# Performance work log

Measured on AMD Instinct MI355X. Metric: run time of the kernel, lower is better.

Reference implementation:

```python
import jax, jax.numpy as jnp
import numpy as np

N = 50000      # nodes
E = 800000     # edges (avg degree 16)
F_IN = 256
F_OUT = 256


def setup_inputs() -> dict:
    key = jax.random.key(0)
    ks = jax.random.split(key, 8)
    feature = jax.random.normal(ks[0], (N, F_IN), dtype=jnp.float32)
    e_w = jax.random.uniform(ks[1], (E, 1), dtype=jnp.float32)
    snorm_n = jnp.ones((N, 1), dtype=jnp.float32)
    snorm_e = jnp.ones((E, 1), dtype=jnp.float32)
    src = jax.random.randint(ks[2], (E,), 0, N, dtype=jnp.int32)
    dst = jax.random.randint(ks[3], (E,), 0, N, dtype=jnp.int32)
    scale = 1.0 / np.sqrt(F_IN)
    W_self = jax.random.normal(ks[4], (F_IN, F_OUT), dtype=jnp.float32) * scale
    W = jax.random.normal(ks[5], (F_IN, F_OUT), dtype=jnp.float32) * scale
    b = jax.random.normal(ks[6], (F_OUT,), dtype=jnp.float32) * scale
    return {"feature": feature, "e_w": e_w, "snorm_n": snorm_n,
            "snorm_e": snorm_e, "W_self": W_self, "W": W, "b": b,
            "src": src, "dst": dst}


def reference(feature, e_w, snorm_n, snorm_e, W_self, W, b, src, dst):
    n = feature.shape[0]
    ones_e = jnp.ones_like(src, dtype=feature.dtype)
    # self transform
    h_s = feature @ W_self                                   # [N, F_OUT]
    # source-side degree normalization: deg_out^{-1/2}
    out_deg = jnp.maximum(jax.ops.segment_sum(ones_e, src, num_segments=n), 1.0)
    feat = feature * (out_deg ** -0.5)[:, None]              # [N, F_IN]
    # message = h[src] * e_w, aggregated by sum into dst (u_mul_e + sum reduce)
    msgs = feat[src] * e_w                                   # [E, F_IN]
    agg = jax.ops.segment_sum(msgs, dst, num_segments=n)     # [N, F_IN]
    # neighbor transform + destination-side degree normalization
    h = agg @ W + b                                          # [N, F_OUT]
    in_deg = jnp.maximum(jax.ops.segment_sum(ones_e, dst, num_segments=n), 1.0)
    h = h * (in_deg ** -0.5)[:, None]
    return h_s + h, e_w
```

## Files before the change

kernel.cpp:

```cpp
#include <hip/hip_runtime.h>
#include <hip/hip_bf16.h>

#define N_NODES 50000
#define N_EDGES 800000
#define MP      50048
#define MAXDEG  64

#define PREP_A_BLOCKS 12512
#define EDGE_BLOCKS   3125
#define PREPW_BLOCKS  512

typedef __bf16 bf16x8_t __attribute__((ext_vector_type(8)));
typedef float  f32x4_t  __attribute__((ext_vector_type(4)));

__device__ __forceinline__ unsigned short f2bf(float x) {
  __hip_bfloat16 h = __float2bfloat16(x);
  return __builtin_bit_cast(unsigned short, h);
}
__device__ __forceinline__ float bf2f(unsigned short u) {
  unsigned int v = ((unsigned int)u) << 16;
  return __builtin_bit_cast(float, v);
}

__global__ __launch_bounds__(256) void prep_fused(
    const float* __restrict__ feature, const float* __restrict__ Wself,
    const float* __restrict__ W, const float* __restrict__ e_w,
    const int* __restrict__ src, const int* __restrict__ dst,
    unsigned short* __restrict__ Abf, unsigned short* __restrict__ Bt,
    int* __restrict__ cnt_in, int* __restrict__ cnt_out,
    unsigned int* __restrict__ bucket, float* __restrict__ out1)
{
  const int b = blockIdx.x, tid = threadIdx.x;
  if (b < PREP_A_BLOCKS) {
    int idx4 = b * 256 + tid;
    size_t base = (size_t)idx4 * 4;
    int row = (int)(base >> 8);
    ushort4 o;
    if (row < N_NODES) {
      const float4 v = *(const float4*)(feature + base);
      o.x = f2bf(v.x); o.y = f2bf(v.y); o.z = f2bf(v.z); o.w = f2bf(v.w);
    } else {
      o.x = o.y = o.z = o.w = 0;
    }
    *(ushort4*)(Abf + base) = o;
  } else if (b < PREP_A_BLOCKS + EDGE_BLOCKS) {
    int e = (b - PREP_A_BLOCKS) * 256 + tid;
    if (e < N_EDGES) {
      int s = src[e];
      int d = dst[e];
      float w = e_w[e];
      out1[e] = w;
      atomicAdd(&cnt_out[s], 1);
      int p = atomicAdd(&cnt_in[d], 1);
      if (p < MAXDEG) {
        unsigned int ent = ((unsigned int)f2bf(w) << 16) | (unsigned int)s;
        bucket[(size_t)d * MAXDEG + p] = ent;
      }
    }
  } else {
    int idx = (b - (PREP_A_BLOCKS + EDGE_BLOCKS)) * 256 + tid;
    int n = idx >> 8, k = idx & 255;
    float v = (n < 256) ? Wself[k * 256 + n] : W[k * 256 + (n - 256)];
    Bt[idx] = f2bf(v);
  }
}

__global__ __launch_bounds__(256, 2) void gemm_kernel(
    const unsigned short* __restrict__ A,
    const unsigned short* __restrict__ Bt,
    const float* __restrict__ bias,
    const int* __restrict__ cnt_in,
    const int* __restrict__ cnt_out,
    float* __restrict__ out0,
    unsigned char* __restrict__ y8)
{
  __shared__ unsigned short As[2][128 * 32];
  __shared__ unsigned short Bs[2][256 * 32];
  const int tid  = threadIdx.x;
  const int lane = tid & 63;
  const int wave = tid >> 6;
  const int m0 = blockIdx.x * 128;
  const int n0 = blockIdx.y * 256;
  const int wm = (wave & 1) * 64;
  const int wn = (wave >> 1) * 128;
  const int fr = lane & 15;
  const int fk = (lane >> 4) * 8;
  const int srow  = lane >> 2;
  const int scolb = (lane & 3) * 8;

  f32x4_t acc[4][8] = {};

  for (int k0 = 0; k0 < 256; k0 += 64) {
#pragma unroll
    for (int p = 0; p < 2; ++p) {
      int kk = k0 + p * 32;
#pragma unroll
      for (int j = 0; j < 2; ++j) {
        int rr = wave * 32 + j * 16;
        const unsigned short* ga = A + (size_t)(m0 + rr + srow) * 256 + (kk + scolb);
        __builtin_amdgcn_global_load_lds((const __attribute__((address_space(1))) void*)ga,
                                         (__attribute__((address_space(3))) void*)&As[p][rr * 32],
                                         16, 0, 0);
      }
#pragma unroll
      for (int j = 0; j < 4; ++j) {
        int rr = wave * 64 + j * 16;
        const unsigned short* gb = Bt + (size_t)(n0 + rr + srow) * 256 + (kk + scolb);
        __builtin_amdgcn_global_load_lds((const __attribute__((address_space(1))) void*)gb,
                                         (__attribute__((address_space(3))) void*)&Bs[p][rr * 32],
                                         16, 0, 0);
      }
    }
    __syncthreads();

#pragma unroll
    for (int p = 0; p < 2; ++p) {
      bf16x8_t af[4], bfr[8];
#pragma unroll
      for (int i = 0; i < 4; ++i)
        af[i]  = *(const bf16x8_t*)&As[p][(wm + i * 16 + fr) * 32 + fk];
#pragma unroll
      for (int j = 0; j < 8; ++j)
        bfr[j] = *(const bf16x8_t*)&Bs[p][(wn + j * 16 + fr) * 32 + fk];
#pragma unroll
      for (int i = 0; i < 4; ++i)
#pragma unroll
        for (int j = 0; j < 8; ++j)
          acc[i][j] = __builtin_amdgcn_mfma_f32_16x16x32_bf16(af[i], bfr[j], acc[i][j], 0, 0, 0);
    }
    __syncthreads();
  }

  if (blockIdx.y == 0) {
#pragma unroll
    for (int i = 0; i < 4; ++i) {
      int rowb = m0 + wm + i * 16 + (lane >> 4) * 4;
      float indv[4];
#pragma unroll
      for (int r = 0; r < 4; ++r) {
        int row = rowb + r;
        if (row < N_NODES) {
          int ci = cnt_in[row]; if (ci < 1) ci = 1;
          indv[r] = rsqrtf((float)ci);
        } else indv[r] = 0.f;
      }
#pragma unroll
      for (int j = 0; j < 8; ++j) {
        int col = wn + j * 16 + (lane & 15);
        float bc = bias[col];
#pragma unroll
        for (int r = 0; r < 4; ++r) {
          int row = rowb + r;
          if (row < N_NODES)
            out0[(size_t)row * 256 + col] = acc[i][j][r] + bc * indv[r];
        }
      }
    }
  } else {
#pragma unroll
    for (int i = 0; i < 4; ++i) {
      int rowb = m0 + wm + i * 16 + (lane >> 4) * 4;
      float odv[4];
#pragma unroll
      for (int r = 0; r < 4; ++r) {
        int row = rowb + r;
        if (row < N_NODES) {
          int co = cnt_out[row]; if (co < 1) co = 1;
          odv[r] = rsqrtf((float)co);
        } else odv[r] = 0.f;
      }
#pragma unroll
      for (int j = 0; j < 8; ++j) {
        int col = wn + j * 16 + (lane & 15);
#pragma unroll
        for (int r = 0; r < 4; ++r) {
          int row = rowb + r;
          if (row < N_NODES) {
            float ys = acc[i][j][r] * odv[r];
            unsigned int pk = (unsigned int)__builtin_amdgcn_cvt_pk_fp8_f32(ys, ys, 0, false);
            y8[(size_t)row * 256 + col] = (unsigned char)(pk & 0xffu);
          }
        }
      }
    }
  }
}

__global__ __launch_bounds__(256) void agg_kernel(
    const unsigned char* __restrict__ y8, const unsigned int* __restrict__ bucket,
    const int* __restrict__ cnt_in, float* __restrict__ out0)
{
  const int wave = threadIdx.x >> 6, lane = threadIdx.x & 63;
  const int node = blockIdx.x * 4 + wave;
  if (node >= N_NODES) return;
  int deg_raw = cnt_in[node];
  int deg = deg_raw > MAXDEG ? MAXDEG : deg_raw;

  unsigned int ent = 0u;
  if (lane < deg) ent = bucket[(size_t)node * MAXDEG + lane];
  float wl = bf2f((unsigned short)(ent >> 16));
  int   sl = (int)(ent & 0xffffu);

  float a0 = 0.f, a1 = 0.f, a2 = 0.f, a3 = 0.f;
  for (int b = 0; b < MAXDEG; b += 16) {
    if (b >= deg) break;
#pragma unroll
    for (int t = 0; t < 16; ++t) {
      int eb = b + t;
      int   s = __shfl(sl, eb);
      float w = __shfl(wl, eb);
      bool ok = eb < deg;
      s = ok ? s : 0;
      w = ok ? w : 0.0f;
      unsigned int u = *(const unsigned int*)(y8 + (size_t)s * 256 + lane * 4);
      a0 += w * __builtin_amdgcn_cvt_f32_fp8(u, 0);
      a1 += w * __builtin_amdgcn_cvt_f32_fp8(u, 1);
      a2 += w * __builtin_amdgcn_cvt_f32_fp8(u, 2);
      a3 += w * __builtin_amdgcn_cvt_f32_fp8(u, 3);
    }
  }

  int dn = deg_raw < 1 ? 1 : deg_raw;
  float inv = rsqrtf((float)dn);
  float4 o = *(float4*)(out0 + (size_t)node * 256 + lane * 4);
  o.x += a0 * inv; o.y += a1 * inv; o.z += a2 * inv; o.w += a3 * inv;
  *(float4*)(out0 + (size_t)node * 256 + lane * 4) = o;
}

extern "C" void kernel_launch(void* const* d_in, const int* in_sizes, int n_in,
                              void* d_out, int out_size, void* d_ws, size_t ws_size,
                              hipStream_t stream) {
  const float* feature = (const float*)d_in[0];
  const float* e_w     = (const float*)d_in[1];
  const float* W_self  = (const float*)d_in[4];
  const float* W       = (const float*)d_in[5];
  const float* bias    = (const float*)d_in[6];
  const int*   src     = (const int*)d_in[7];
  const int*   dst     = (const int*)d_in[8];

  float* out0 = (float*)d_out;
  float* out1 = out0 + (size_t)N_NODES * 256;

  char* ws = (char*)d_ws;
  int*            cnt_in  = (int*)(ws + 0);
  int*            cnt_out = (int*)(ws + 204800);
  unsigned int*   bucket  = (unsigned int*)(ws + 409600);
  unsigned short* Bt      = (unsigned short*)(ws + 13209600);
  unsigned short* Abf     = (unsigned short*)(ws + 13471744);
  unsigned char*  y8      = (unsigned char*)(ws + 39096320);

  hipMemsetAsync(ws, 0, 409600, stream);

  prep_fused<<<PREP_A_BLOCKS + EDGE_BLOCKS + PREPW_BLOCKS, 256, 0, stream>>>(
      feature, W_self, W, e_w, src, dst, Abf, Bt, cnt_in, cnt_out, bucket, out1);
  gemm_kernel<<<dim3(MP / 128, 2), 256, 0, stream>>>(Abf, Bt, bias, cnt_in, cnt_out, out0, y8);
  agg_kernel<<<(N_NODES + 3) / 4, 256, 0, stream>>>(y8, bucket, cnt_in, out0);
}
```

Baseline: 265.3 us.

## Fuse bf16 feature conversion into GEMM and co-schedule edge bucketing blocks

```diff
diff --git a/kernel.cpp b/kernel.cpp
--- a/kernel.cpp
+++ b/kernel.cpp
@@ -6,9 +6,9 @@
 #define MP      50048
 #define MAXDEG  64
 
-#define PREP_A_BLOCKS 12512
-#define EDGE_BLOCKS   3125
-#define PREPW_BLOCKS  512
+#define GEMM_BLOCKS  782
+#define EDGE_BLOCKS  782
+#define WCONV_BLOCKS 512
 
 typedef __bf16 bf16x8_t __attribute__((ext_vector_type(8)));
 typedef float  f32x4_t  __attribute__((ext_vector_type(4)));
@@ -22,86 +22,71 @@
   return __builtin_bit_cast(float, v);
 }
 
-__global__ __launch_bounds__(256) void prep_fused(
-    const float* __restrict__ feature, const float* __restrict__ Wself,
-    const float* __restrict__ W, const float* __restrict__ e_w,
-    const int* __restrict__ src, const int* __restrict__ dst,
-    unsigned short* __restrict__ Abf, unsigned short* __restrict__ Bt,
+__global__ __launch_bounds__(256) void wconv_kernel(
+    const float* __restrict__ Wself, const float* __restrict__ W,
+    unsigned short* __restrict__ Bt)
+{
+  int idx = blockIdx.x * 256 + threadIdx.x;
+  int n = idx >> 8, k = idx & 255;
+  float v = (n < 256) ? Wself[k * 256 + n] : W[k * 256 + (n - 256)];
+  Bt[idx] = f2bf(v);
+}
+
+__global__ __launch_bounds__(256, 2) void gemm_edge_kernel(
+    const float* __restrict__ feature,
+    const unsigned short* __restrict__ Bt,
+    const float* __restrict__ e_w, const int* __restrict__ src, const int* __restrict__ dst,
     int* __restrict__ cnt_in, int* __restrict__ cnt_out,
-    unsigned int* __restrict__ bucket, float* __restrict__ out1)
-{
-  const int b = blockIdx.x, tid = threadIdx.x;
-  if (b < PREP_A_BLOCKS) {
-    int idx4 = b * 256 + tid;
-    size_t base = (size_t)idx4 * 4;
-    int row = (int)(base >> 8);
-    ushort4 o;
-    if (row < N_NODES) {
-      const float4 v = *(const float4*)(feature + base);
-      o.x = f2bf(v.x); o.y = f2bf(v.y); o.z = f2bf(v.z); o.w = f2bf(v.w);
-    } else {
-      o.x = o.y = o.z = o.w = 0;
-    }
-    *(ushort4*)(Abf + base) = o;
-  } else if (b < PREP_A_BLOCKS + EDGE_BLOCKS) {
-    int e = (b - PREP_A_BLOCKS) * 256 + tid;
-    if (e < N_EDGES) {
-      int s = src[e];
-      int d = dst[e];
-      float w = e_w[e];
-      out1[e] = w;
-      atomicAdd(&cnt_out[s], 1);
-      int p = atomicAdd(&cnt_in[d], 1);
-      if (p < MAXDEG) {
-        unsigned int ent = ((unsigned int)f2bf(w) << 16) | (unsigned int)s;
-        bucket[(size_t)d * MAXDEG + p] = ent;
-      }
-    }
-  } else {
-    int idx = (b - (PREP_A_BLOCKS + EDGE_BLOCKS)) * 256 + tid;
-    int n = idx >> 8, k = idx & 255;
-    float v = (n < 256) ? Wself[k * 256 + n] : W[k * 256 + (n - 256)];
-    Bt[idx] = f2bf(v);
-  }
-}
-
-__global__ __launch_bounds__(256, 2) void gemm_kernel(
-    const unsigned short* __restrict__ A,
-    const unsigned short* __restrict__ Bt,
-    const float* __restrict__ bias,
-    const int* __restrict__ cnt_in,
-    const int* __restrict__ cnt_out,
+    unsigned int* __restrict__ bucket, float* __restrict__ out1,
     float* __restrict__ out0,
     unsigned char* __restrict__ y8)
 {
-  __shared__ unsigned short As[2][128 * 32];
-  __shared__ unsigned short Bs[2][256 * 32];
-  const int tid  = threadIdx.x;
+  const int b   = blockIdx.x;
+  const int tid = threadIdx.x;
+
+  if (b & 1) {
+    const int e0 = (b >> 1) * 1024 + tid;
+#pragma unroll
+    for (int k = 0; k < 4; ++k) {
+      int e = e0 + k * 256;
+      if (e < N_EDGES) {
+        int s = src[e];
+        int d = dst[e];
+        float w = e_w[e];
+        out1[e] = w;
+        atomicAdd(&cnt_out[s], 1);
+        int p = atomicAdd(&cnt_in[d], 1);
+        if (p < MAXDEG) {
+          unsigned int ent = ((unsigned int)f2bf(w) << 16) | (unsigned int)s;
+          bucket[(size_t)d * MAXDEG + p] = ent;
+        }
+      }
+    }
+    return;
+  }
+
+  __shared__ __align__(16) unsigned short As[2][128 * 32];
+  __shared__ __align__(16) unsigned short Bs[2][256 * 32];
+  const int g    = b >> 1;
+  const int half = g & 1;
+  const int m0   = (g >> 1) * 128;
+  const int n0   = half * 256;
   const int lane = tid & 63;
   const int wave = tid >> 6;
-  const int m0 = blockIdx.x * 128;
-  const int n0 = blockIdx.y * 256;
   const int wm = (wave & 1) * 64;
   const int wn = (wave >> 1) * 128;
   const int fr = lane & 15;
   const int fk = (lane >> 4) * 8;
   const int srow  = lane >> 2;
   const int scolb = (lane & 3) * 8;
+  const bool full = (m0 + 128) <= N_NODES;
 
   f32x4_t acc[4][8] = {};
 
   for (int k0 = 0; k0 < 256; k0 += 64) {
 #pragma unroll
     for (int p = 0; p < 2; ++p) {
-      int kk = k0 + p * 32;
-#pragma unroll
-      for (int j = 0; j < 2; ++j) {
-        int rr = wave * 32 + j * 16;
-        const unsigned short* ga = A + (size_t)(m0 + rr + srow) * 256 + (kk + scolb);
-        __builtin_amdgcn_global_load_lds((const __attribute__((address_space(1))) void*)ga,
-                                         (__attribute__((address_space(3))) void*)&As[p][rr * 32],
-                                         16, 0, 0);
-      }
+      const int kk = k0 + p * 32;
 #pragma unroll
       for (int j = 0; j < 4; ++j) {
         int rr = wave * 64 + j * 16;
@@ -110,6 +95,23 @@
                                          (__attribute__((address_space(3))) void*)&Bs[p][rr * 32],
                                          16, 0, 0);
       }
+#pragma unroll
+      for (int j = 0; j < 2; ++j) {
+        const int rr   = wave * 32 + j * 16 + srow;
+        const int grow = m0 + rr;
+        float4 v0 = {0.f, 0.f, 0.f, 0.f}, v1 = {0.f, 0.f, 0.f, 0.f};
+        if (full || grow < N_NODES) {
+          const float* ga = feature + (size_t)grow * 256 + (kk + scolb);
+          v0 = *(const float4*)ga;
+          v1 = *(const float4*)(ga + 4);
+        }
+        uint4 pk;
+        pk.x = ((unsigned int)f2bf(v0.y) << 16) | (unsigned int)f2bf(v0.x);
+        pk.y = ((unsigned int)f2bf(v0.w) << 16) | (unsigned int)f2bf(v0.z);
+        pk.z = ((unsigned int)f2bf(v1.y) << 16) | (unsigned int)f2bf(v1.x);
+        pk.w = ((unsigned int)f2bf(v1.w) << 16) | (unsigned int)f2bf(v1.z);
+        *(uint4*)&As[p][rr * 32 + scolb] = pk;
+      }
     }
     __syncthreads();
 
@@ -131,28 +133,18 @@
     __syncthreads();
   }
 
-  if (blockIdx.y == 0) {
+  if (half == 0) {
 #pragma unroll
     for (int i = 0; i < 4; ++i) {
       int rowb = m0 + wm + i * 16 + (lane >> 4) * 4;
-      float indv[4];
-#pragma unroll
-      for (int r = 0; r < 4; ++r) {
-        int row = rowb + r;
-        if (row < N_NODES) {
-          int ci = cnt_in[row]; if (ci < 1) ci = 1;
-          indv[r] = rsqrtf((float)ci);
-        } else indv[r] = 0.f;
-      }
 #pragma unroll
       for (int j = 0; j < 8; ++j) {
         int col = wn + j * 16 + (lane & 15);
-        float bc = bias[col];
 #pragma unroll
         for (int r = 0; r < 4; ++r) {
           int row = rowb + r;
           if (row < N_NODES)
-            out0[(size_t)row * 256 + col] = acc[i][j][r] + bc * indv[r];
+            out0[(size_t)row * 256 + col] = acc[i][j][r];
         }
       }
     }
@@ -160,15 +152,6 @@
 #pragma unroll
     for (int i = 0; i < 4; ++i) {
       int rowb = m0 + wm + i * 16 + (lane >> 4) * 4;
-      float odv[4];
-#pragma unroll
-      for (int r = 0; r < 4; ++r) {
-        int row = rowb + r;
-        if (row < N_NODES) {
-          int co = cnt_out[row]; if (co < 1) co = 1;
-          odv[r] = rsqrtf((float)co);
-        } else odv[r] = 0.f;
-      }
 #pragma unroll
       for (int j = 0; j < 8; ++j) {
         int col = wn + j * 16 + (lane & 15);
@@ -176,7 +159,7 @@
         for (int r = 0; r < 4; ++r) {
           int row = rowb + r;
           if (row < N_NODES) {
-            float ys = acc[i][j][r] * odv[r];
+            float ys = acc[i][j][r];
             unsigned int pk = (unsigned int)__builtin_amdgcn_cvt_pk_fp8_f32(ys, ys, 0, false);
             y8[(size_t)row * 256 + col] = (unsigned char)(pk & 0xffu);
           }
@@ -188,7 +171,8 @@
 
 __global__ __launch_bounds__(256) void agg_kernel(
     const unsigned char* __restrict__ y8, const unsigned int* __restrict__ bucket,
-    const int* __restrict__ cnt_in, float* __restrict__ out0)
+    const int* __restrict__ cnt_in, const int* __restrict__ cnt_out,
+    const float* __restrict__ bias, float* __restrict__ out0)
 {
   const int wave = threadIdx.x >> 6, lane = threadIdx.x & 63;
   const int node = blockIdx.x * 4 + wave;
@@ -198,15 +182,17 @@
 
   unsigned int ent = 0u;
   if (lane < deg) ent = bucket[(size_t)node * MAXDEG + lane];
+  int   sl = (int)(ent & 0xffffu);
   float wl = bf2f((unsigned short)(ent >> 16));
-  int   sl = (int)(ent & 0xffffu);
+  int co = cnt_out[sl]; if (co < 1) co = 1;
+  wl *= rsqrtf((float)co);
 
   float a0 = 0.f, a1 = 0.f, a2 = 0.f, a3 = 0.f;
-  for (int b = 0; b < MAXDEG; b += 16) {
-    if (b >= deg) break;
+  for (int bb = 0; bb < MAXDEG; bb += 16) {
+    if (bb >= deg) break;
 #pragma unroll
     for (int t = 0; t < 16; ++t) {
-      int eb = b + t;
+      int eb = bb + t;
       int   s = __shfl(sl, eb);
       float w = __shfl(wl, eb);
       bool ok = eb < deg;
@@ -222,8 +208,12 @@
 
   int dn = deg_raw < 1 ? 1 : deg_raw;
   float inv = rsqrtf((float)dn);
+  float4 bc = *(const float4*)(bias + lane * 4);
   float4 o = *(float4*)(out0 + (size_t)node * 256 + lane * 4);
-  o.x += a0 * inv; o.y += a1 * inv; o.z += a2 * inv; o.w += a3 * inv;
+  o.x += (a0 + bc.x) * inv;
+  o.y += (a1 + bc.y) * inv;
+  o.z += (a2 + bc.z) * inv;
+  o.w += (a3 + bc.w) * inv;
   *(float4*)(out0 + (size_t)node * 256 + lane * 4) = o;
 }
 
@@ -246,13 +236,12 @@
   int*            cnt_out = (int*)(ws + 204800);
   unsigned int*   bucket  = (unsigned int*)(ws + 409600);
   unsigned short* Bt      = (unsigned short*)(ws + 13209600);
-  unsigned short* Abf     = (unsigned short*)(ws + 13471744);
-  unsigned char*  y8      = (unsigned char*)(ws + 39096320);
+  unsigned char*  y8      = (unsigned char*)(ws + 13471744);
 
   hipMemsetAsync(ws, 0, 409600, stream);
 
-  prep_fused<<<PREP_A_BLOCKS + EDGE_BLOCKS + PREPW_BLOCKS, 256, 0, stream>>>(
-      feature, W_self, W, e_w, src, dst, Abf, Bt, cnt_in, cnt_out, bucket, out1);
-  gemm_kernel<<<dim3(MP / 128, 2), 256, 0, stream>>>(Abf, Bt, bias, cnt_in, cnt_out, out0, y8);
-  agg_kernel<<<(N_NODES + 3) / 4, 256, 0, stream>>>(y8, bucket, cnt_in, out0);
-}
+  wconv_kernel<<<WCONV_BLOCKS, 256, 0, stream>>>(W_self, W, Bt);
+  gemm_edge_kernel<<<GEMM_BLOCKS + EDGE_BLOCKS, 256, 0, stream>>>(
+      feature, Bt, e_w, src, dst, cnt_in, cnt_out, bucket, out1, out0, y8);
+  agg_kernel<<<(N_NODES + 3) / 4, 256, 0, stream>>>(y8, bucket, cnt_in, cnt_out, bias, out0);
+}
```

New measurement: 260.5 us. Within noise of the previous version (-1.8%).
